# Optimization experiments

Hardware: AMD Instinct MI355X
Metric: run time of the kernel (lower is better)

## Reference

```python
import jax, jax.numpy as jnp
import numpy as np

N_NODES = 50000
N_EDGES = 800000
D_IN, D_HID, D_OUT = 256, 128, 64
NEG_SLOPE = 0.2  # PyG GATConv default


def gat_conv(x, W, a_src, a_dst, b, src, dst, n):
    """Single-head PyG-style GATConv with self-loops already in (src, dst)."""
    h = x @ W                                  # [N, d_out]
    # per-edge attention logits: LeakyReLU(a_src . h_src + a_dst . h_dst)
    e = jax.nn.leaky_relu((h @ a_src)[src] + (h @ a_dst)[dst], NEG_SLOPE)  # [E]
    # segment softmax over incoming edges of each dst node (stable)
    e = e - jax.ops.segment_max(e, dst, num_segments=n)[dst]
    p = jnp.exp(e)
    p = p / jax.ops.segment_sum(p, dst, num_segments=n)[dst]
    # weighted scatter-add of source messages
    out = jax.ops.segment_sum(p[:, None] * h[src], dst, num_segments=n)
    return out + b


def setup_inputs() -> dict:
    key = jax.random.key(0)
    ks = jax.random.split(key, 10)
    x = jax.random.normal(ks[0], (N_NODES, D_IN), dtype=jnp.float32)
    edge_index = jax.random.randint(ks[1], (2, N_EDGES), 0, N_NODES, dtype=jnp.int32)
    s1 = 1.0 / np.sqrt(D_IN)
    s2 = 1.0 / np.sqrt(D_HID)
    W1 = jax.random.normal(ks[2], (D_IN, D_HID), dtype=jnp.float32) * s1
    a_src1 = jax.random.normal(ks[3], (D_HID,), dtype=jnp.float32) * s2
    a_dst1 = jax.random.normal(ks[4], (D_HID,), dtype=jnp.float32) * s2
    b1 = jnp.zeros((D_HID,), dtype=jnp.float32)
    W2 = jax.random.normal(ks[5], (D_HID, D_OUT), dtype=jnp.float32) * s2
    a_src2 = jax.random.normal(ks[6], (D_OUT,), dtype=jnp.float32) * (1.0 / np.sqrt(D_OUT))
    a_dst2 = jax.random.normal(ks[7], (D_OUT,), dtype=jnp.float32) * (1.0 / np.sqrt(D_OUT))
    b2 = jnp.zeros((D_OUT,), dtype=jnp.float32)
    return {"x": x, "edge_index": edge_index, "W1": W1, "a_src1": a_src1,
            "a_dst1": a_dst1, "b1": b1, "W2": W2, "a_src2": a_src2,
            "a_dst2": a_dst2, "b2": b2}


def reference(x, edge_index, W1, a_src1, a_dst1, b1, W2, a_src2, a_dst2, b2):
    n = x.shape[0]
    loops = jnp.arange(n, dtype=edge_index.dtype)
    src = jnp.concatenate([edge_index[0], loops])  # add_self_loops=True (PyG default)
    dst = jnp.concatenate([edge_index[1], loops])
    h = gat_conv(x, W1, a_src1, a_dst1, b1, src, dst, n)
    h = jax.nn.relu(h)
    return gat_conv(h, W2, a_src2, a_dst2, b2, src, dst, n)
```

## Files before the change

kernel.cpp:

```cpp
#include <hip/hip_runtime.h>
#include <stdint.h>

#define DIN 256
#define DHID 128
#define DOUTD 64
#define NBLK 128
#define BCAP 4096

typedef __attribute__((ext_vector_type(8))) short bf16x8;
typedef __attribute__((ext_vector_type(4))) float f32x4;

__device__ __forceinline__ uint32_t pack_bf16x2(float x, float y) {
    uint32_t ux = __builtin_bit_cast(uint32_t, x);
    uint32_t uy = __builtin_bit_cast(uint32_t, y);
    ux += 0x7fffu + ((ux >> 16) & 1u);
    uy += 0x7fffu + ((uy >> 16) & 1u);
    return (ux >> 16) | (uy & 0xffff0000u);
}
__device__ __forceinline__ uint16_t to_bf16(float x) {
    uint32_t u = __builtin_bit_cast(uint32_t, x);
    u += 0x7fffu + ((u >> 16) & 1u);
    return (uint16_t)(u >> 16);
}
__device__ __forceinline__ float bflo(uint32_t v) { return __builtin_bit_cast(float, v << 16); }
__device__ __forceinline__ float bfhi(uint32_t v) { return __builtin_bit_cast(float, v & 0xffff0000u); }

template<int K, int N>
__device__ __forceinline__ void prepack_body(
    const float* __restrict__ W, uint16_t* __restrict__ Bp, int t)
{
    constexpr int CB = N / 16;
    if (t >= (K / 32) * CB * 64) return;
    const int lane = t & 63, fi = t >> 6;
    const int c = fi % CB, kb = fi / CB;
    const int j  = 16 * c + (lane & 15);
    const int k0 = kb * 32 + (lane >> 4) * 8;
    uint32_t o[4];
    #pragma unroll
    for (int i = 0; i < 4; ++i) {
        float lo = W[(size_t)(k0 + 2 * i)     * N + j];
        float hi = W[(size_t)(k0 + 2 * i + 1) * N + j];
        o[i] = pack_bf16x2(lo, hi);
    }
    *reinterpret_cast<uint4*>(&Bp[(size_t)t * 8]) = make_uint4(o[0], o[1], o[2], o[3]);
}

__global__ __launch_bounds__(256) void prepack_both_kernel(
    const float* __restrict__ W1, uint16_t* __restrict__ Bp1,
    const float* __restrict__ W2, uint16_t* __restrict__ Bp2,
    int* __restrict__ cntG, int nbuck)
{
    if (blockIdx.x == 0) {
        for (int i = threadIdx.x; i < nbuck; i += 256) cntG[i] = 0;
    }
    if (blockIdx.x < 16)
        prepack_body<DIN, DHID>(W1, Bp1, blockIdx.x * 256 + threadIdx.x);
    else
        prepack_body<DHID, DOUTD>(W2, Bp2, (blockIdx.x - 16) * 256 + threadIdx.x);
}

template<int K, int N, bool AF32>
__device__ __forceinline__ void gemm_body(
    uint16_t* __restrict__ As,
    const void* __restrict__ A, const uint16_t* __restrict__ Bp,
    uint16_t* __restrict__ Cout, const float* __restrict__ a_s,
    const float* __restrict__ a_d, float* __restrict__ asrc,
    float* __restrict__ adst, int M, int bid)
{
    constexpr int KB = K / 32, CB = N / 16;
    const int tid = threadIdx.x;
    const int row0 = bid * 64;

    if (AF32) {
        constexpr int NIT = 64 * K / 4 / 256;
        #pragma unroll
        for (int i = 0; i < NIT; ++i) {
            int u = tid + i * 256;
            int row = u / (K / 4);
            int k4  = (u % (K / 4)) * 4;
            float4 v = make_float4(0.f, 0.f, 0.f, 0.f);
            if (row0 + row < M)
                v = *reinterpret_cast<const float4*>((const float*)A + (size_t)(row0 + row) * K + k4);
            uint32_t byte = (uint32_t)row * (K * 2) + k4 * 2;
            byte ^= (row & 7) << 4;
            *reinterpret_cast<uint2*>((char*)As + byte) =
                make_uint2(pack_bf16x2(v.x, v.y), pack_bf16x2(v.z, v.w));
        }
    } else {
        constexpr int NIT = 64 * K / 8 / 256;
        #pragma unroll
        for (int i = 0; i < NIT; ++i) {
            int u = tid + i * 256;
            int row = u / (K / 8);
            int k8  = (u % (K / 8)) * 8;
            uint4 v = make_uint4(0u, 0u, 0u, 0u);
            if (row0 + row < M)
                v = *reinterpret_cast<const uint4*>((const uint16_t*)A + (size_t)(row0 + row) * K + k8);
            uint32_t byte = (uint32_t)row * (K * 2) + k8 * 2;
            byte ^= (row & 7) << 4;
            *reinterpret_cast<uint4*>((char*)As + byte) = v;
        }
    }
    __syncthreads();

    const int w = tid >> 6, l = tid & 63;
    const int rA = w * 16 + (l & 15);

    f32x4 acc[CB] = {};
    const char* blane = (const char*)Bp + l * 16;

    #pragma unroll
    for (int kb = 0; kb < KB; ++kb) {
        uint32_t abyte = (uint32_t)rA * (K * 2) + (kb * 32 + (l >> 4) * 8) * 2;
        abyte ^= (rA & 7) << 4;
        bf16x8 a = *reinterpret_cast<const bf16x8*>((const char*)As + abyte);
        #pragma unroll
        for (int c = 0; c < CB; ++c) {
            bf16x8 b = *reinterpret_cast<const bf16x8*>(blane + (size_t)(kb * CB + c) * 1024);
            acc[c] = __builtin_amdgcn_mfma_f32_16x16x32_bf16(a, b, acc[c], 0, 0, 0);
        }
    }

    const int rb = w * 16 + (l >> 4) * 4;
    const int colb = l & 15;

    #pragma unroll
    for (int c = 0; c < CB; ++c) {
        #pragma unroll
        for (int r = 0; r < 4; ++r) {
            int grow = row0 + rb + r;
            if (grow < M)
                Cout[(size_t)grow * N + c * 16 + colb] = to_bf16(acc[c][r]);
        }
    }

    float ps[4] = {}, pd[4] = {};
    #pragma unroll
    for (int c = 0; c < CB; ++c) {
        float asv = a_s[c * 16 + colb];
        float adv = a_d[c * 16 + colb];
        #pragma unroll
        for (int r = 0; r < 4; ++r) {
            ps[r] += acc[c][r] * asv;
            pd[r] += acc[c][r] * adv;
        }
    }
    #pragma unroll
    for (int mask = 1; mask < 16; mask <<= 1) {
        #pragma unroll
        for (int r = 0; r < 4; ++r) {
            ps[r] += __shfl_xor(ps[r], mask);
            pd[r] += __shfl_xor(pd[r], mask);
        }
    }
    if (colb == 0) {
        #pragma unroll
        for (int r = 0; r < 4; ++r) {
            int grow = row0 + rb + r;
            if (grow < M) { asrc[grow] = ps[r]; adst[grow] = pd[r]; }
        }
    }
}

__global__ __launch_bounds__(256) void hybrid_kernel(
    const int* __restrict__ ei, int E, int n, int nbuck, int chunk,
    int* __restrict__ cntG, uint32_t* __restrict__ bucketed,
    const float* __restrict__ x, const uint16_t* __restrict__ Bp1,
    uint16_t* __restrict__ Hb, const float* __restrict__ a_s,
    const float* __restrict__ a_d, float* __restrict__ asrc,
    float* __restrict__ adst)
{
    __shared__ __align__(16) uint16_t As[64 * DIN];
    __shared__ int h[512];
    __shared__ int curL[512];

    if (blockIdx.x < NBLK) {
        for (int i = threadIdx.x; i < nbuck; i += 256) h[i] = 0;
        __syncthreads();
        const int blk = blockIdx.x;
        const int ET = E + n;
        const int e0 = blk * chunk, e1 = min(e0 + chunk, ET);
        for (int e = e0 + threadIdx.x; e < e1; e += 256) {
            int d = (e < E) ? ei[E + e] : (e - E);
            atomicAdd(&h[d >> 7], 1);
        }
        __syncthreads();
        for (int i = threadIdx.x; i < nbuck; i += 256) {
            int c = h[i];
            int base = i * BCAP;
            if (c) base += atomicAdd(&cntG[i], c);
            curL[i] = base;
        }
        __syncthreads();
        for (int e = e0 + threadIdx.x; e < e1; e += 256) {
            int s, d;
            if (e < E) { s = ei[e]; d = ei[E + e]; }
            else       { s = e - E; d = s; }
            int pos = atomicAdd(&curL[d >> 7], 1);
            bucketed[pos] = ((uint32_t)d << 16) | (uint32_t)s;
        }
    } else {
        gemm_body<DIN, DHID, true>(As, x, Bp1, Hb, a_s, a_d, asrc, adst, n,
                                   blockIdx.x - NBLK);
    }
}

__global__ __launch_bounds__(256) void gemm2_kernel(
    const uint16_t* __restrict__ A, const uint16_t* __restrict__ Bp,
    uint16_t* __restrict__ Cout, const float* __restrict__ a_s,
    const float* __restrict__ a_d, float* __restrict__ asrc,
    float* __restrict__ adst, int M)
{
    __shared__ __align__(16) uint16_t As[64 * DHID];
    gemm_body<DHID, DOUTD, false>(As, A, Bp, Cout, a_s, a_d, asrc, adst, M,
                                  blockIdx.x);
}

template<int D, bool RELU, bool OUTB16>
__global__ __launch_bounds__(1024) void aggF_kernel(
    const uint32_t* __restrict__ bucketed, const int* __restrict__ cntG,
    const uint32_t* __restrict__ Hb, const float* __restrict__ asrc,
    const float* __restrict__ adst, const float* __restrict__ bias,
    void* __restrict__ out, int n)
{
    constexpr int C16 = D / 8;
    constexpr int EPI = 64 / C16;
    __shared__ uint16_t csr_l[BCAP];
    __shared__ int hist[128];
    __shared__ int scn[128];
    __shared__ int offs_l[128];
    __shared__ int cur[128];

    const int b = blockIdx.x;
    const int tid = threadIdx.x;
    const int bbase = b * BCAP;
    const int cnt = cntG[b];

    if (tid < 128) hist[tid] = 0;
    __syncthreads();
    for (int i = tid; i < cnt; i += 1024)
        atomicAdd(&hist[(bucketed[bbase + i] >> 16) & 127], 1);
    __syncthreads();
    if (tid < 128) scn[tid] = hist[tid];
    __syncthreads();
    #pragma unroll
    for (int off = 1; off < 128; off <<= 1) {
        int v = (tid < 128 && tid >= off) ? scn[tid - off] : 0;
        __syncthreads();
        if (tid < 128) scn[tid] += v;
        __syncthreads();
    }
    if (tid < 128) {
        int excl = scn[tid] - hist[tid];
        offs_l[tid] = excl;
        cur[tid] = excl;
    }
    __syncthreads();
    for (int i = tid; i < cnt; i += 1024) {
        uint32_t pk = bucketed[bbase + i];
        int pos = atomicAdd(&cur[(pk >> 16) & 127], 1);
        csr_l[pos] = (uint16_t)(pk & 0xFFFFu);
    }
    __syncthreads();

    const int wv = tid >> 6, lane = tid & 63;
    const int seg = lane / C16;
    const int chk = lane & (C16 - 1);
    const uint4* __restrict__ H4 = reinterpret_cast<const uint4*>(Hb);

    for (int j = 0; j < 8; ++j) {
        const int ln = wv + 16 * j;
        const int node = b * 128 + ln;
        if (node >= n) continue;
        const int beg = offs_l[ln];
        const int deg = hist[ln];
        const float ad = adst[node];

        float acc[8] = {};
        float ssum = 0.f;

        for (int base = 0; base < deg; base += 64) {
            const int lim = min(64, deg - base);
            float wt = 0.f; int st = 0;
            if (lane < lim) {
                st = csr_l[beg + base + lane];
                float t = asrc[st] + ad;
                t = (t > 0.f) ? t : 0.2f * t;
                wt = __expf(t);
            }
            ssum += wt;
            const int iters = (lim + 2 * EPI - 1) / (2 * EPI);
            #pragma unroll 2
            for (int it = 0; it < iters; ++it) {
                int e0 = it * 2 * EPI + seg;
                int e1 = e0 + EPI;
                float w0 = __shfl(wt, e0);
                int   s0 = __shfl(st, e0);
                float w1 = __shfl(wt, e1);
                int   s1 = __shfl(st, e1);
                uint4 v0 = H4[(size_t)s0 * (D / 8) + chk];
                uint4 v1 = H4[(size_t)s1 * (D / 8) + chk];
                acc[0] += w0 * bflo(v0.x); acc[1] += w0 * bfhi(v0.x);
                acc[2] += w0 * bflo(v0.y); acc[3] += w0 * bfhi(v0.y);
                acc[4] += w0 * bflo(v0.z); acc[5] += w0 * bfhi(v0.z);
                acc[6] += w0 * bflo(v0.w); acc[7] += w0 * bfhi(v0.w);
                acc[0] += w1 * bflo(v1.x); acc[1] += w1 * bfhi(v1.x);
                acc[2] += w1 * bflo(v1.y); acc[3] += w1 * bfhi(v1.y);
                acc[4] += w1 * bflo(v1.z); acc[5] += w1 * bfhi(v1.z);
                acc[6] += w1 * bflo(v1.w); acc[7] += w1 * bfhi(v1.w);
            }
        }

        #pragma unroll
        for (int mask = C16; mask < 64; mask <<= 1)
            #pragma unroll
            for (int q = 0; q < 8; ++q)
                acc[q] += __shfl_xor(acc[q], mask);
        #pragma unroll
        for (int off = 32; off; off >>= 1) ssum += __shfl_xor(ssum, off);
        const float inv = 1.f / ssum;

        if (seg == 0) {
            const int col0 = chk * 8;
            float r[8];
            #pragma unroll
            for (int q = 0; q < 8; ++q) {
                r[q] = acc[q] * inv + bias[col0 + q];
                if (RELU) r[q] = fmaxf(r[q], 0.f);
            }
            if (OUTB16) {
                uint4 o = make_uint4(pack_bf16x2(r[0], r[1]), pack_bf16x2(r[2], r[3]),
                                     pack_bf16x2(r[4], r[5]), pack_bf16x2(r[6], r[7]));
                *(reinterpret_cast<uint4*>(out) + (size_t)node * (D / 8) + chk) = o;
            } else {
                float* op = (float*)out + (size_t)node * D + col0;
                *reinterpret_cast<float4*>(op)     = make_float4(r[0], r[1], r[2], r[3]);
                *reinterpret_cast<float4*>(op + 4) = make_float4(r[4], r[5], r[6], r[7]);
            }
        }
    }
}

extern "C" void kernel_launch(void* const* d_in, const int* in_sizes, int n_in,
                              void* d_out, int out_size, void* d_ws, size_t ws_size,
                              hipStream_t stream)
{
    const float* x   = (const float*)d_in[0];
    const int*   ei  = (const int*)  d_in[1];
    const float* W1  = (const float*)d_in[2];
    const float* as1 = (const float*)d_in[3];
    const float* ad1 = (const float*)d_in[4];
    const float* b1  = (const float*)d_in[5];
    const float* W2  = (const float*)d_in[6];
    const float* as2 = (const float*)d_in[7];
    const float* ad2 = (const float*)d_in[8];
    const float* b2  = (const float*)d_in[9];
    float* out = (float*)d_out;

    const int n  = in_sizes[0] / DIN;
    const int E  = in_sizes[1] / 2;
    const int ET = E + n;

    const int nbuck  = (n + 127) >> 7;
    const int chunk  = (ET + NBLK - 1) / NBLK;

    char* ws = (char*)d_ws;
    size_t off = 0;
    auto alloc = [&](size_t bytes) -> void* {
        off = (off + 255) & ~(size_t)255;
        void* p = ws + off;
        off += bytes;
        return p;
    };
    uint16_t* Hb   = (uint16_t*)alloc((size_t)n * DHID * 2);
    uint16_t* O1b  = (uint16_t*)alloc((size_t)n * DHID * 2);
    uint16_t* H2b  = (uint16_t*)alloc((size_t)n * DOUTD * 2);
    float* asrc    = (float*)alloc((size_t)n * 4);
    float* adst    = (float*)alloc((size_t)n * 4);
    uint16_t* Bp1  = (uint16_t*)alloc((size_t)DIN * DHID * 2);
    uint16_t* Bp2  = (uint16_t*)alloc((size_t)DHID * DOUTD * 2);
    int* cntG  = (int*)alloc((size_t)nbuck * 4);
    uint32_t* bucketed = (uint32_t*)alloc((size_t)nbuck * BCAP * 4);

    const int ng = (n + 63) / 64;

    prepack_both_kernel<<<20, 256, 0, stream>>>(W1, Bp1, W2, Bp2, cntG, nbuck);

    hybrid_kernel<<<NBLK + ng, 256, 0, stream>>>(
        ei, E, n, nbuck, chunk, cntG, bucketed,
        x, Bp1, Hb, as1, ad1, asrc, adst);

    aggF_kernel<DHID, true, true><<<nbuck, 1024, 0, stream>>>(
        bucketed, cntG, (const uint32_t*)Hb, asrc, adst, b1, O1b, n);

    gemm2_kernel<<<ng, 256, 0, stream>>>(O1b, Bp2, H2b, as2, ad2, asrc, adst, n);

    aggF_kernel<DOUTD, false, false><<<nbuck, 1024, 0, stream>>>(
        bucketed, cntG, (const uint32_t*)H2b, asrc, adst, b2, out, n);
}
```

Baseline: 209.4 us.

## Shrink aggregation buckets to 32 nodes and split hybrid kernel into separate launches

Bucket granularity drops from 128 to 32 destination nodes per bucket, and each aggregation block shrinks to 256 threads. This gives many more, smaller blocks, to improve load balance and occupancy and to cut LDS use in the per-bucket CSR build. The fused histogram/GEMM hybrid kernel is split into a standalone histogram-scatter kernel and a GEMM1 kernel. That removes the overlap the fused launch gave but allows the larger bucket table. The extra launch and more global atomics on cntG are the cost, and bucket capacity 1024 assumes no 32-node bucket overflows.

```diff
diff --git a/kernel.cpp b/kernel.cpp
--- a/kernel.cpp
+++ b/kernel.cpp
@@ -5,7 +5,10 @@
 #define DHID 128
 #define DOUTD 64
 #define NBLK 128
-#define BCAP 4096
+#define BSH 5
+#define BNODES 32
+#define BCAP 1024
+#define MAXBUCK 2048
 
 typedef __attribute__((ext_vector_type(8))) short bf16x8;
 typedef __attribute__((ext_vector_type(4))) float f32x4;
@@ -162,47 +165,14 @@
     }
 }
 
-__global__ __launch_bounds__(256) void hybrid_kernel(
-    const int* __restrict__ ei, int E, int n, int nbuck, int chunk,
-    int* __restrict__ cntG, uint32_t* __restrict__ bucketed,
-    const float* __restrict__ x, const uint16_t* __restrict__ Bp1,
-    uint16_t* __restrict__ Hb, const float* __restrict__ a_s,
+__global__ __launch_bounds__(256) void gemm1_kernel(
+    const float* __restrict__ A, const uint16_t* __restrict__ Bp,
+    uint16_t* __restrict__ Cout, const float* __restrict__ a_s,
     const float* __restrict__ a_d, float* __restrict__ asrc,
-    float* __restrict__ adst)
+    float* __restrict__ adst, int M)
 {
     __shared__ __align__(16) uint16_t As[64 * DIN];
-    __shared__ int h[512];
-    __shared__ int curL[512];
-
-    if (blockIdx.x < NBLK) {
-        for (int i = threadIdx.x; i < nbuck; i += 256) h[i] = 0;
-        __syncthreads();
-        const int blk = blockIdx.x;
-        const int ET = E + n;
-        const int e0 = blk * chunk, e1 = min(e0 + chunk, ET);
-        for (int e = e0 + threadIdx.x; e < e1; e += 256) {
-            int d = (e < E) ? ei[E + e] : (e - E);
-            atomicAdd(&h[d >> 7], 1);
-        }
-        __syncthreads();
-        for (int i = threadIdx.x; i < nbuck; i += 256) {
-            int c = h[i];
-            int base = i * BCAP;
-            if (c) base += atomicAdd(&cntG[i], c);
-            curL[i] = base;
-        }
-        __syncthreads();
-        for (int e = e0 + threadIdx.x; e < e1; e += 256) {
-            int s, d;
-            if (e < E) { s = ei[e]; d = ei[E + e]; }
-            else       { s = e - E; d = s; }
-            int pos = atomicAdd(&curL[d >> 7], 1);
-            bucketed[pos] = ((uint32_t)d << 16) | (uint32_t)s;
-        }
-    } else {
-        gemm_body<DIN, DHID, true>(As, x, Bp1, Hb, a_s, a_d, asrc, adst, n,
-                                   blockIdx.x - NBLK);
-    }
+    gemm_body<DIN, DHID, true>(As, A, Bp, Cout, a_s, a_d, asrc, adst, M, blockIdx.x);
 }
 
 __global__ __launch_bounds__(256) void gemm2_kernel(
@@ -212,12 +182,43 @@
     float* __restrict__ adst, int M)
 {
     __shared__ __align__(16) uint16_t As[64 * DHID];
-    gemm_body<DHID, DOUTD, false>(As, A, Bp, Cout, a_s, a_d, asrc, adst, M,
-                                  blockIdx.x);
+    gemm_body<DHID, DOUTD, false>(As, A, Bp, Cout, a_s, a_d, asrc, adst, M, blockIdx.x);
+}
+
+__global__ __launch_bounds__(256) void histscatter_kernel(
+    const int* __restrict__ ei, int E, int n, int nbuck, int chunk,
+    int* __restrict__ cntG, uint32_t* __restrict__ bucketed)
+{
+    __shared__ int h[MAXBUCK];
+    __shared__ int curL[MAXBUCK];
+    for (int i = threadIdx.x; i < nbuck; i += 256) h[i] = 0;
+    __syncthreads();
+    const int blk = blockIdx.x;
+    const int ET = E + n;
+    const int e0 = blk * chunk, e1 = min(e0 + chunk, ET);
+    for (int e = e0 + threadIdx.x; e < e1; e += 256) {
+        int d = (e < E) ? ei[E + e] : (e - E);
+        atomicAdd(&h[d >> BSH], 1);
+    }
+    __syncthreads();
+    for (int i = threadIdx.x; i < nbuck; i += 256) {
+        int c = h[i];
+        int base = i * BCAP;
+        if (c) base += atomicAdd(&cntG[i], c);
+        curL[i] = base;
+    }
+    __syncthreads();
+    for (int e = e0 + threadIdx.x; e < e1; e += 256) {
+        int s, d;
+        if (e < E) { s = ei[e]; d = ei[E + e]; }
+        else       { s = e - E; d = s; }
+        int pos = atomicAdd(&curL[d >> BSH], 1);
+        bucketed[pos] = ((uint32_t)d << 16) | (uint32_t)s;
+    }
 }
 
 template<int D, bool RELU, bool OUTB16>
-__global__ __launch_bounds__(1024) void aggF_kernel(
+__global__ __launch_bounds__(256) void aggF_kernel(
     const uint32_t* __restrict__ bucketed, const int* __restrict__ cntG,
     const uint32_t* __restrict__ Hb, const float* __restrict__ asrc,
     const float* __restrict__ adst, const float* __restrict__ bias,
@@ -226,39 +227,39 @@
     constexpr int C16 = D / 8;
     constexpr int EPI = 64 / C16;
     __shared__ uint16_t csr_l[BCAP];
-    __shared__ int hist[128];
-    __shared__ int scn[128];
-    __shared__ int offs_l[128];
-    __shared__ int cur[128];
+    __shared__ int hist[BNODES];
+    __shared__ int scn[BNODES];
+    __shared__ int offs_l[BNODES];
+    __shared__ int cur[BNODES];
 
     const int b = blockIdx.x;
     const int tid = threadIdx.x;
     const int bbase = b * BCAP;
     const int cnt = cntG[b];
 
-    if (tid < 128) hist[tid] = 0;
-    __syncthreads();
-    for (int i = tid; i < cnt; i += 1024)
-        atomicAdd(&hist[(bucketed[bbase + i] >> 16) & 127], 1);
-    __syncthreads();
-    if (tid < 128) scn[tid] = hist[tid];
-    __syncthreads();
-    #pragma unroll
-    for (int off = 1; off < 128; off <<= 1) {
-        int v = (tid < 128 && tid >= off) ? scn[tid - off] : 0;
+    if (tid < BNODES) hist[tid] = 0;
+    __syncthreads();
+    for (int i = tid; i < cnt; i += 256)
+        atomicAdd(&hist[(bucketed[bbase + i] >> 16) & (BNODES - 1)], 1);
+    __syncthreads();
+    if (tid < BNODES) scn[tid] = hist[tid];
+    __syncthreads();
+    #pragma unroll
+    for (int off = 1; off < BNODES; off <<= 1) {
+        int v = (tid < BNODES && tid >= off) ? scn[tid - off] : 0;
         __syncthreads();
-        if (tid < 128) scn[tid] += v;
+        if (tid < BNODES) scn[tid] += v;
         __syncthreads();
     }
-    if (tid < 128) {
+    if (tid < BNODES) {
         int excl = scn[tid] - hist[tid];
         offs_l[tid] = excl;
         cur[tid] = excl;
     }
     __syncthreads();
-    for (int i = tid; i < cnt; i += 1024) {
+    for (int i = tid; i < cnt; i += 256) {
         uint32_t pk = bucketed[bbase + i];
-        int pos = atomicAdd(&cur[(pk >> 16) & 127], 1);
+        int pos = atomicAdd(&cur[(pk >> 16) & (BNODES - 1)], 1);
         csr_l[pos] = (uint16_t)(pk & 0xFFFFu);
     }
     __syncthreads();
@@ -269,8 +270,8 @@
     const uint4* __restrict__ H4 = reinterpret_cast<const uint4*>(Hb);
 
     for (int j = 0; j < 8; ++j) {
-        const int ln = wv + 16 * j;
-        const int node = b * 128 + ln;
+        const int ln = wv + 4 * j;
+        const int node = b * BNODES + ln;
         if (node >= n) continue;
         const int beg = offs_l[ln];
         const int deg = hist[ln];
@@ -361,7 +362,7 @@
     const int E  = in_sizes[1] / 2;
     const int ET = E + n;
 
-    const int nbuck  = (n + 127) >> 7;
+    const int nbuck  = (n + BNODES - 1) >> BSH;
     const int chunk  = (ET + NBLK - 1) / NBLK;
 
     char* ws = (char*)d_ws;
@@ -386,15 +387,15 @@
 
     prepack_both_kernel<<<20, 256, 0, stream>>>(W1, Bp1, W2, Bp2, cntG, nbuck);
 
-    hybrid_kernel<<<NBLK + ng, 256, 0, stream>>>(
-        ei, E, n, nbuck, chunk, cntG, bucketed,
-        x, Bp1, Hb, as1, ad1, asrc, adst);
-
-    aggF_kernel<DHID, true, true><<<nbuck, 1024, 0, stream>>>(
+    histscatter_kernel<<<NBLK, 256, 0, stream>>>(ei, E, n, nbuck, chunk, cntG, bucketed);
+
+    gemm1_kernel<<<ng, 256, 0, stream>>>(x, Bp1, Hb, as1, ad1, asrc, adst, n);
+
+    aggF_kernel<DHID, true, true><<<nbuck, 256, 0, stream>>>(
         bucketed, cntG, (const uint32_t*)Hb, asrc, adst, b1, O1b, n);
 
     gemm2_kernel<<<ng, 256, 0, stream>>>(O1b, Bp2, H2b, as2, ad2, asrc, adst, n);
 
-    aggF_kernel<DOUTD, false, false><<<nbuck, 1024, 0, stream>>>(
+    aggF_kernel<DOUTD, false, false><<<nbuck, 256, 0, stream>>>(
         bucketed, cntG, (const uint32_t*)H2b, asrc, adst, b2, out, n);
 }
```

Measured after the change: 219.7 us. 4.9% more time.
